# Kernel optimization log

Measured on AMD Instinct MI355X. Metric: run time of the kernel, lower is better.

## Reference

```python
import jax, jax.numpy as jnp
import numpy as np

B, D, L, T, K = 16, 256, 256, 1000, 3
DW, DC = 4, 2  # dim_w, dim_c
CH = 8         # ConvSwishBlock out channels (10 = 1 start + 1 end + 8)


def swish(x):
    return x * jax.nn.sigmoid(x)


def setup_inputs() -> dict:
    key = jax.random.key(0)
    ks = jax.random.split(key, 12)
    # durations ~ U[1,6] per phone -> sum ~ 3.5*L ~ 896 <= T
    durations = 1.0 + 5.0 * jax.random.uniform(ks[0], (B, L), dtype=jnp.float32)
    phoneme = jax.random.normal(ks[1], (B, D, L), dtype=jnp.float32)
    # True = padded phone position
    phone_len = L - (jnp.arange(B) % 4) * 16
    phoneme_mask = (jnp.arange(L)[None, :] >= phone_len[:, None])[:, None, :]
    durations = jnp.where(phoneme_mask[:, 0, :], 0.0, durations)
    s = 0.02
    p = {
        'proj_w_W': s * jax.random.normal(ks[2], (D, D)), 'proj_w_b': jnp.zeros((D,)),
        'conv_w_W': s * jax.random.normal(ks[3], (CH, D, K)), 'conv_w_b': jnp.zeros((CH,)),
        'mlp_w_W': s * jax.random.normal(ks[4], (2 + CH, DW)), 'mlp_w_b': jnp.zeros((DW,)),
        'lin_w_W': s * jax.random.normal(ks[5], (D * DW, D)), 'lin_w_b': jnp.zeros((D,)),
        'proj_c_W': s * jax.random.normal(ks[6], (D, D)), 'proj_c_b': jnp.zeros((D,)),
        'conv_c_W': s * jax.random.normal(ks[7], (CH, D, K)), 'conv_c_b': jnp.zeros((CH,)),
        'mlp_c_W': s * jax.random.normal(ks[8], (2 + CH, DC)), 'mlp_c_b': jnp.zeros((DC,)),
        'lin_c_W': s * jax.random.normal(ks[9], (DW * DC, D)), 'lin_c_b': jnp.zeros((D,)),
    }
    return {'durations': durations, 'phoneme': phoneme, 'phoneme_mask': phoneme_mask, **p}


def _conv_branch(x, phone_pad, projW, projb, convW, convb):
    # x: (B, D, L). 1x1 conv projection, then K-wide 'same' conv to CH channels, swish, mask.
    x = jnp.einsum('od,bdl->bol', projW, x) + projb[None, :, None]
    h = jax.lax.conv_general_dilated(x, convW, (1,), 'SAME',
                                     dimension_numbers=('NCH', 'OIH', 'NCH'))
    h = swish(h + convb[None, :, None])
    h = jnp.where(phone_pad[:, None, :], 0.0, h)
    return h.transpose(0, 2, 1)  # (B, L, CH)


def _forward(durations, phoneme, phoneme_mask,
             proj_w_W, proj_w_b, conv_w_W, conv_w_b, mlp_w_W, mlp_w_b, lin_w_W, lin_w_b,
             proj_c_W, proj_c_b, conv_c_W, conv_c_b, mlp_c_W, mlp_c_b, lin_c_W, lin_c_b):
    phone_pad = phoneme_mask[:, 0, :]                       # (B, L) True = pad
    frame_len = jnp.clip(jnp.round(jnp.sum(durations, -1)), 0, T).astype(jnp.int32)
    frame_pad = jnp.arange(T)[None, :] >= frame_len[:, None]  # (B, T) True = pad
    attn_pad = frame_pad[:, :, None] | phone_pad[:, None, :]  # (B, T, L)

    sd = jnp.cumsum(durations, -1)                          # (B, L) cumulative end times
    sk = sd - durations                                     # (B, L) start times
    t = jnp.arange(1, T + 1, dtype=durations.dtype)
    S = jnp.where(attn_pad, 0.0, t[None, :, None] - sk[:, None, :])                    # (B,T,L)
    E = jnp.where(attn_pad, 0.0, jnp.broadcast_to(sd[:, None, :], attn_pad.shape)
                  - sk[:, None, :])                                                    # (B,T,L)

    # W branch: per-(frame, phone) attention weights over phones
    h_w = _conv_branch(phoneme, phone_pad, proj_w_W, proj_w_b, conv_w_W, conv_w_b)     # (B,L,CH)
    feat_w = jnp.concatenate(
        [S[..., None], E[..., None], jnp.broadcast_to(h_w[:, None], (B, T, L, CH))], -1)
    w = swish(feat_w @ mlp_w_W + mlp_w_b)                   # (B, T, L, DW)
    w = jnp.where(phone_pad[:, None, :, None], -jnp.inf, w)
    w = jax.nn.softmax(w, axis=2)                           # softmax over phones
    w = jnp.where(frame_pad[:, :, None, None], 0.0, w)

    # C branch: auxiliary per-(frame, phone) context
    h_c = _conv_branch(phoneme, phone_pad, proj_c_W, proj_c_b, conv_c_W, conv_c_b)
    feat_c = jnp.concatenate(
        [S[..., None], E[..., None], jnp.broadcast_to(h_c[:, None], (B, T, L, CH))], -1)
    c = swish(feat_c @ mlp_c_W + mlp_c_b)                   # (B, T, L, DC)

    # combine: wh = einsum over phones with phoneme features, wc with c matrix
    wh = jnp.einsum('btnq,bnh->btqh', w, phoneme.transpose(0, 2, 1))  # (B,T,DW,D)
    wh = wh.reshape(B, T, DW * D) @ lin_w_W + lin_w_b                 # (B,T,D)
    wc = jnp.einsum('btnq,btnp->btqp', w, c)                          # (B,T,DW,DC)
    wc = wc.reshape(B, T, DW * DC) @ lin_c_W + lin_c_b                # (B,T,D)
    return wh + wc


def reference(durations, phoneme, phoneme_mask,
              proj_w_W, proj_w_b, conv_w_W, conv_w_b, mlp_w_W, mlp_w_b, lin_w_W, lin_w_b,
              proj_c_W, proj_c_b, conv_c_W, conv_c_b, mlp_c_W, mlp_c_b, lin_c_W, lin_c_b):
    return _forward(durations, phoneme, phoneme_mask,
                    proj_w_W, proj_w_b, conv_w_W, conv_w_b, mlp_w_W, mlp_w_b, lin_w_W, lin_w_b,
                    proj_c_W, proj_c_b, conv_c_W, conv_c_b, mlp_c_W, mlp_c_b, lin_c_W, lin_c_b)
```

## Files before the change

### kernel.cpp

```cpp
#include <hip/hip_runtime.h>


typedef short v8s __attribute__((ext_vector_type(8)));
typedef _Float16 v8h __attribute__((ext_vector_type(8)));
typedef float f4 __attribute__((ext_vector_type(4)));

__device__ __forceinline__ float bf2f(unsigned short h) {
  return __uint_as_float(((unsigned int)h) << 16);
}
__device__ __forceinline__ unsigned short f2bf(float f) {
  unsigned int u = __float_as_uint(f);
  u = (u + 0x7FFFu + ((u >> 16) & 1u)) >> 16;
  return (unsigned short)u;
}
__device__ __forceinline__ float swishf(float x) {
  return x * __builtin_amdgcn_rcpf(1.f + __expf(-x));
}

__global__ __launch_bounds__(256) void k_prep(
    const float* __restrict__ dur, const float* __restrict__ ph,
    const float* __restrict__ liWw,
    const float* __restrict__ cvWw, const float* __restrict__ pjWw,
    const float* __restrict__ pjbw,
    const float* __restrict__ cvWc, const float* __restrict__ pjWc,
    const float* __restrict__ pjbc,
    float* __restrict__ sk, int* __restrict__ frame_len,
    unsigned short* __restrict__ Mb, float* __restrict__ bK,
    unsigned short* __restrict__ LWT, unsigned short* __restrict__ phT) {
  __shared__ float sm[32 * 33];
  int blk = blockIdx.x, tid = threadIdx.x;
  if (blk < 16) {
    int b = blk, l = tid;
    float d = dur[b * 256 + l];
    sm[l] = d;
    __syncthreads();
    for (int off = 1; off < 256; off <<= 1) {
      float v = (l >= off) ? sm[l - off] : 0.f;
      __syncthreads();
      sm[l] += v;
      __syncthreads();
    }
    sk[b * 256 + l] = sm[l] - d;
    if (l == 255) {
      int fl = (int)rintf(sm[255]);
      frame_len[b] = min(max(fl, 0), 1000);
    }
  } else if (blk < 64) {
    int x = blk - 16;
    int br = x / 24, ck = x % 24;
    int ch = ck / 3, k = ck % 3;
    const float* convW = br ? cvWc : cvWw;
    const float* projW = br ? pjWc : pjWw;
    const float* projb = br ? pjbc : pjbw;
    int d = tid;
    float acc = 0.f;
    for (int o = 0; o < 256; o++)
      acc += convW[ch * 768 + o * 3 + k] * projW[o * 256 + d];
    Mb[(br * 24 + ck) * 256 + d] = f2bf(acc);
    if (d == 0) {
      float bb = 0.f;
      for (int o = 0; o < 256; o++)
        bb += convW[ch * 768 + o * 3 + k] * projb[o];
      bK[br * 24 + ck] = bb;
    }
  } else if (blk < 320) {
    int idx = blk - 64;
    int kt = idx & 31, ot = idx >> 5;
    int tx = tid & 31, ty = tid >> 5;
#pragma unroll
    for (int r = 0; r < 4; r++) {
      int row = ty + r * 8;
      sm[row * 33 + tx] = liWw[(size_t)(kt * 32 + row) * 256 + ot * 32 + tx];
    }
    __syncthreads();
#pragma unroll
    for (int r = 0; r < 4; r++) {
      int row = ty + r * 8;
      LWT[(size_t)(ot * 32 + row) * 1024 + kt * 32 + tx] =
          f2bf(sm[tx * 33 + row]);
    }
  } else {
    int idx = blk - 320;
    int ht = idx & 7, lt = (idx >> 3) & 7, b = idx >> 6;
    int tx = tid & 31, ty = tid >> 5;
#pragma unroll
    for (int r = 0; r < 4; r++) {
      int row = ty + r * 8;
      sm[row * 33 + tx] =
          ph[(size_t)b * 65536 + (size_t)(ht * 32 + row) * 256 + lt * 32 + tx];
    }
    __syncthreads();
#pragma unroll
    for (int r = 0; r < 4; r++) {
      int row = ty + r * 8;
      phT[(size_t)b * 65536 + (size_t)(lt * 32 + row) * 256 + ht * 32 + tx] =
          f2bf(sm[tx * 33 + row]);
    }
  }
}

__global__ __launch_bounds__(256) void k_convG(
    const unsigned short* __restrict__ phT, const unsigned short* __restrict__ Mb,
    const float* __restrict__ bK, const float* __restrict__ cvbw,
    const float* __restrict__ cvbc, const float* __restrict__ dur,
    const unsigned short* __restrict__ LWT,
    float* __restrict__ hw, float* __restrict__ hc,
    _Float16* __restrict__ G) {
  __shared__ __align__(16) char smem[50176];
  int blk = blockIdx.x;
  int tid = threadIdx.x, wave = tid >> 6, lane = tid & 63;
  int quad = lane >> 4, col = lane & 15;
  if (blk < 16) {
    float* C = (float*)smem;
    int b = blk;
    int l0 = wave * 64;
    const unsigned short* Ab = phT + (size_t)b * 65536;
    f4 acc[4][3] = {};
#pragma unroll
    for (int k0 = 0; k0 < 256; k0 += 32) {
      v8s af[4], bf[3];
#pragma unroll
      for (int lt = 0; lt < 4; lt++)
        af[lt] = *(const v8s*)(Ab + (size_t)(l0 + lt * 16 + col) * 256 + k0 + quad * 8);
#pragma unroll
      for (int ct = 0; ct < 3; ct++)
        bf[ct] = *(const v8s*)(Mb + (size_t)(ct * 16 + col) * 256 + k0 + quad * 8);
#pragma unroll
      for (int lt = 0; lt < 4; lt++)
#pragma unroll
        for (int ct = 0; ct < 3; ct++)
          acc[lt][ct] = __builtin_amdgcn_mfma_f32_16x16x32_bf16(af[lt], bf[ct],
                                                                acc[lt][ct], 0, 0, 0);
    }
#pragma unroll
    for (int lt = 0; lt < 4; lt++)
#pragma unroll
      for (int ct = 0; ct < 3; ct++)
#pragma unroll
        for (int r = 0; r < 4; r++)
          C[(l0 + lt * 16 + quad * 4 + r) * 49 + ct * 16 + col] = acc[lt][ct][r];
    __syncthreads();
    int l = tid;
    float dv = dur[b * 256 + l];
    bool vld = (dv != 0.f);
#pragma unroll
    for (int br = 0; br < 2; br++) {
      const float* convb = br ? cvbc : cvbw;
      float* dst = br ? hc : hw;
#pragma unroll
      for (int ch = 0; ch < 8; ch++) {
        int ck = br * 24 + ch * 3;
        float v = convb[ch] + bK[ck + 1] + C[l * 49 + ck + 1];
        if (l > 0) v += bK[ck + 0] + C[(l - 1) * 49 + ck + 0];
        if (l < 255) v += bK[ck + 2] + C[(l + 1) * 49 + ck + 2];
        v = swishf(v);
        dst[((size_t)(b * 256 + l)) * 8 + ch] = vld ? v : 0.f;
      }
    }
  } else {
    int idx = blk - 16;
    int x = idx & 7, q = (idx >> 3) & 3, b = idx >> 5;
    int o0 = (x >> 1) * 64, l0 = (x & 1) * 128;
    unsigned short* Asm = (unsigned short*)smem;
    unsigned short* Bsm = Asm + 64 * 40;
    int arow = wave * 16 + (lane >> 2);
    int aseg = lane & 3;
    const unsigned short* Ag = LWT + (size_t)(o0 + arow) * 1024 + q * 256 + aseg * 8;
    unsigned short* Al = Asm + arow * 40 + aseg * 8;
    int brow = wave * 32 + (lane >> 2);
    const unsigned short* Bg0 =
        phT + (size_t)b * 65536 + (size_t)(l0 + brow) * 256 + aseg * 8;
    const unsigned short* Bg1 = Bg0 + 16 * 256;
    unsigned short* Bl0 = Bsm + brow * 40 + aseg * 8;
    unsigned short* Bl1 = Bl0 + 16 * 40;
    int wm = (wave & 1) * 32, wn = (wave >> 1) * 64;
    f4 acc[2][4] = {};
    uint4 ra = *(const uint4*)Ag;
    uint4 rb0 = *(const uint4*)Bg0;
    uint4 rb1 = *(const uint4*)Bg1;
    for (int k0 = 0; k0 < 256; k0 += 32) {
      __syncthreads();
      *(uint4*)Al = ra;
      *(uint4*)Bl0 = rb0;
      *(uint4*)Bl1 = rb1;
      __syncthreads();
      if (k0 + 32 < 256) {
        ra = *(const uint4*)(Ag + k0 + 32);
        rb0 = *(const uint4*)(Bg0 + k0 + 32);
        rb1 = *(const uint4*)(Bg1 + k0 + 32);
      }
      v8s af[2], bf[4];
#pragma unroll
      for (int mt = 0; mt < 2; mt++)
        af[mt] = *(const v8s*)(Asm + (wm + mt * 16 + col) * 40 + quad * 8);
#pragma unroll
      for (int nt = 0; nt < 4; nt++)
        bf[nt] = *(const v8s*)(Bsm + (wn + nt * 16 + col) * 40 + quad * 8);
#pragma unroll
      for (int mt = 0; mt < 2; mt++)
#pragma unroll
        for (int nt = 0; nt < 4; nt++)
          acc[mt][nt] = __builtin_amdgcn_mfma_f32_16x16x32_bf16(af[mt], bf[nt],
                                                                acc[mt][nt], 0, 0, 0);
    }
#pragma unroll
    for (int mt = 0; mt < 2; mt++)
#pragma unroll
      for (int nt = 0; nt < 4; nt++)
#pragma unroll
        for (int r = 0; r < 4; r++) {
          int orow = o0 + wm + mt * 16 + quad * 4 + r;
          int lcol = l0 + wn + nt * 16 + col;
          G[(size_t)b * 262144 + (size_t)orow * 1024 + q * 256 + lcol] =
              (_Float16)acc[mt][nt][r];
        }
  }
}

__global__ __launch_bounds__(256) void k_fuse(
    const _Float16* __restrict__ G,
    const float* __restrict__ dur, const float* __restrict__ sk,
    const int* __restrict__ frame_len,
    const float* __restrict__ hw, const float* __restrict__ hc,
    const float* __restrict__ mlpWw, const float* __restrict__ mlpbw,
    const float* __restrict__ mlpWc, const float* __restrict__ mlpbc,
    const float* __restrict__ lwb, const float* __restrict__ lcb,
    const float* __restrict__ LC, float* __restrict__ out) {
  __shared__ __align__(16) _Float16 Et[2][32][264];
  __shared__ __align__(16) float4 Lbw4[256];
  __shared__ __align__(16) float4 Laux4[256];
  __shared__ float4 wredM[4];
  __shared__ float invL[32 * 4];
  __shared__ float wcL[32 * 8];

  int blk = blockIdx.x;
  int b = (blk & 7) * 2 + ((blk >> 3) & 1);
  int tile = blk >> 4;
  int t0 = tile * 32;
  int tid = threadIdx.x, wave = tid >> 6, lane = tid & 63;
  int quad = lane >> 4, col = lane & 15;

  {
    int l = tid;
    float4 a0 = *(const float4*)&hw[((size_t)(b * 256 + l)) * 8];
    float4 a1 = *(const float4*)&hw[((size_t)(b * 256 + l)) * 8 + 4];
    float4 c0 = *(const float4*)&hc[((size_t)(b * 256 + l)) * 8];
    float4 c1 = *(const float4*)&hc[((size_t)(b * 256 + l)) * 8 + 4];
    float hwv[8] = {a0.x, a0.y, a0.z, a0.w, a1.x, a1.y, a1.z, a1.w};
    float hcv[8] = {c0.x, c0.y, c0.z, c0.w, c1.x, c1.y, c1.z, c1.w};
    float dl = dur[b * 256 + l];
    float skl = sk[b * 256 + l];
    float msk = (dl != 0.f) ? 1.f : 0.f;
    float A[4];
#pragma unroll
    for (int q = 0; q < 4; q++) {
      float a = mlpbw[q] + dl * mlpWw[4 + q] - skl * mlpWw[q];
#pragma unroll
      for (int ch = 0; ch < 8; ch++) a += hwv[ch] * mlpWw[(2 + ch) * 4 + q];
      A[q] = (msk != 0.f) ? a : -1e30f;
    }
    float bb0 = mlpbc[0] + dl * mlpWc[2] - skl * mlpWc[0];
    float bb1 = mlpbc[1] + dl * mlpWc[3] - skl * mlpWc[1];
#pragma unroll
    for (int ch = 0; ch < 8; ch++) {
      bb0 += hcv[ch] * mlpWc[(2 + ch) * 2 + 0];
      bb1 += hcv[ch] * mlpWc[(2 + ch) * 2 + 1];
    }
    float4 Av = {A[0], A[1], A[2], A[3]};
    Lbw4[l] = Av;
    float4 xv = {bb0, bb1, msk, 0.f};
    Laux4[l] = xv;
    float m0 = A[0], m1 = A[1], m2 = A[2], m3 = A[3];
#pragma unroll
    for (int off = 1; off < 64; off <<= 1) {
      m0 = fmaxf(m0, __shfl_xor(m0, off));
      m1 = fmaxf(m1, __shfl_xor(m1, off));
      m2 = fmaxf(m2, __shfl_xor(m2, off));
      m3 = fmaxf(m3, __shfl_xor(m3, off));
    }
    if (lane == 0) {
      float4 mv = {m0, m1, m2, m3};
      wredM[wave] = mv;
    }
  }
  __syncthreads();
  float4 W0 = wredM[0], W1 = wredM[1], W2 = wredM[2], W3 = wredM[3];
  float maxA[4] = {fmaxf(fmaxf(W0.x, W1.x), fmaxf(W2.x, W3.x)),
                   fmaxf(fmaxf(W0.y, W1.y), fmaxf(W2.y, W3.y)),
                   fmaxf(fmaxf(W0.z, W1.z), fmaxf(W2.z, W3.z)),
                   fmaxf(fmaxf(W0.w, W1.w), fmaxf(W2.w, W3.w))};

  int fl = frame_len[b];
  int tg = tid >> 5, seg = tid & 31;
  float mw0[4] = {mlpWw[0], mlpWw[1], mlpWw[2], mlpWw[3]};
  float mc0 = mlpWc[0], mc1 = mlpWc[1];
  float tp1v[4], tS0[4], tS1[4];
  bool livev[4];
#pragma unroll
  for (int ti = 0; ti < 4; ti++) {
    int t = t0 + tg * 4 + ti;
    livev[ti] = (t < fl);
    tp1v[ti] = (float)(t + 1);
    tS0[ti] = tp1v[ti] * mc0;
    tS1[ti] = tp1v[ti] * mc1;
  }

  int wn = wave * 64;
  f4 accF[2][4] = {};
  const _Float16* Gb = G + (size_t)b * 262144;

#pragma unroll
  for (int pp = 0; pp < 2; pp++) {
    if (pp) __syncthreads();
    int qa = pp * 2;
    float mm[4][2];
#pragma unroll
    for (int ti = 0; ti < 4; ti++) {
      mm[ti][0] = livev[ti] ? fmaxf(maxA[qa] + tp1v[ti] * mw0[qa], 0.f) : 1e30f;
      mm[ti][1] = livev[ti] ? fmaxf(maxA[qa + 1] + tp1v[ti] * mw0[qa + 1], 0.f) : 1e30f;
    }
    float s[4][2] = {}, pw0[4][2] = {}, pw1[4][2] = {};
    for (int jj = 0; jj < 8; jj++) {
      int l = jj * 32 + seg;
      float4 A4 = Lbw4[l];
      float4 ax = Laux4[l];
      float Aa = pp ? A4.z : A4.x;
      float Ab = pp ? A4.w : A4.y;
#pragma unroll
      for (int ti = 0; ti < 4; ti++) {
        float tp1 = tp1v[ti];
        float za = Aa + tp1 * mw0[qa];
        float zb = Ab + tp1 * mw0[qa + 1];
        float ea = __expf(swishf(za) - mm[ti][0]) * ax.z;
        float eb = __expf(swishf(zb) - mm[ti][1]) * ax.z;
        float cp0 = swishf(ax.x + tS0[ti]);
        float cp1 = swishf(ax.y + tS1[ti]);
        s[ti][0] += ea;  pw0[ti][0] += ea * cp0;  pw1[ti][0] += ea * cp1;
        s[ti][1] += eb;  pw0[ti][1] += eb * cp0;  pw1[ti][1] += eb * cp1;
        Et[0][tg * 4 + ti][l] = (_Float16)ea;
        Et[1][tg * 4 + ti][l] = (_Float16)eb;
      }
    }
#pragma unroll
    for (int off = 1; off < 32; off <<= 1) {
#pragma unroll
      for (int ti = 0; ti < 4; ti++) {
#pragma unroll
        for (int e2 = 0; e2 < 2; e2++) {
          s[ti][e2] += __shfl_xor(s[ti][e2], off);
          pw0[ti][e2] += __shfl_xor(pw0[ti][e2], off);
          pw1[ti][e2] += __shfl_xor(pw1[ti][e2], off);
        }
      }
    }
    if (seg == 0) {
#pragma unroll
      for (int ti = 0; ti < 4; ti++) {
        int row = tg * 4 + ti;
#pragma unroll
        for (int e2 = 0; e2 < 2; e2++) {
          int qq = qa + e2;
          float iv = livev[ti] ? __builtin_amdgcn_rcpf(s[ti][e2]) : 0.f;
          invL[row * 4 + qq] = iv;
          wcL[row * 8 + qq * 2 + 0] = pw0[ti][e2] * iv;
          wcL[row * 8 + qq * 2 + 1] = pw1[ti][e2] * iv;
        }
      }
    }
    __syncthreads();
#pragma unroll
    for (int e2 = 0; e2 < 2; e2++) {
      int qq = qa + e2;
      f4 accq[2][4] = {};
#pragma unroll
      for (int k0 = 0; k0 < 256; k0 += 32) {
        v8h af[2], bf[4];
#pragma unroll
        for (int mt = 0; mt < 2; mt++)
          af[mt] = *(const v8h*)&Et[e2][mt * 16 + col][k0 + quad * 8];
#pragma unroll
        for (int nt = 0; nt < 4; nt++)
          bf[nt] = *(const v8h*)(Gb + (size_t)(wn + nt * 16 + col) * 1024 +
                                 qq * 256 + k0 + quad * 8);
#pragma unroll
        for (int mt = 0; mt < 2; mt++)
#pragma unroll
          for (int nt = 0; nt < 4; nt++)
            accq[mt][nt] = __builtin_amdgcn_mfma_f32_16x16x32_f16(af[mt], bf[nt],
                                                                  accq[mt][nt], 0, 0, 0);
      }
#pragma unroll
      for (int mt = 0; mt < 2; mt++)
#pragma unroll
        for (int r = 0; r < 4; r++) {
          float iv = invL[(mt * 16 + quad * 4 + r) * 4 + qq];
#pragma unroll
          for (int nt = 0; nt < 4; nt++)
            accF[mt][nt][r] += accq[mt][nt][r] * iv;
        }
    }
  }

#pragma unroll
  for (int nt = 0; nt < 4; nt++) {
    int oc = wn + nt * 16 + col;
    float bias = lwb[oc] + lcb[oc];
    float lc8[8];
#pragma unroll
    for (int jj = 0; jj < 8; jj++) lc8[jj] = LC[jj * 256 + oc];
#pragma unroll
    for (int mt = 0; mt < 2; mt++)
#pragma unroll
      for (int r = 0; r < 4; r++) {
        int lr = mt * 16 + quad * 4 + r;
        int trow = t0 + lr;
        if (trow < 1000) {
          float v = accF[mt][nt][r] + bias;
#pragma unroll
          for (int jj = 0; jj < 8; jj++) v = fmaf(wcL[lr * 8 + jj], lc8[jj], v);
          out[((size_t)(b * 1000 + trow)) * 256 + oc] = v;
        }
      }
  }
}

extern "C" void kernel_launch(void* const* d_in, const int* in_sizes, int n_in,
                              void* d_out, int out_size, void* d_ws, size_t ws_size,
                              hipStream_t stream) {
  const float* dur  = (const float*)d_in[0];
  const float* ph   = (const float*)d_in[1];
  const float* pjWw = (const float*)d_in[3];
  const float* pjbw = (const float*)d_in[4];
  const float* cvWw = (const float*)d_in[5];
  const float* cvbw = (const float*)d_in[6];
  const float* mlWw = (const float*)d_in[7];
  const float* mlbw = (const float*)d_in[8];
  const float* liWw = (const float*)d_in[9];
  const float* libw = (const float*)d_in[10];
  const float* pjWc = (const float*)d_in[11];
  const float* pjbc = (const float*)d_in[12];
  const float* cvWc = (const float*)d_in[13];
  const float* cvbc = (const float*)d_in[14];
  const float* mlWc = (const float*)d_in[15];
  const float* mlbc = (const float*)d_in[16];
  const float* liWc = (const float*)d_in[17];
  const float* libc = (const float*)d_in[18];
  float* out = (float*)d_out;

  float* f = (float*)d_ws;
  size_t o = 0;
  float* sk = f + o;            o += 4096;
  int* fl = (int*)(f + o);      o += 16;
  float* bK = f + o;            o += 64;
  unsigned short* Mb = (unsigned short*)(f + o); o += 6144;
  float* hw = f + o;            o += 16 * 256 * 8;
  float* hc = f + o;            o += 16 * 256 * 8;
  _Float16* G = (_Float16*)(f + o);              o += 2097152;
  unsigned short* phT = (unsigned short*)(f + o); o += 524288;
  unsigned short* LWT = (unsigned short*)(f + o); o += 131072;

  k_prep<<<1344, 256, 0, stream>>>(dur, ph, liWw, cvWw, pjWw, pjbw, cvWc, pjWc,
                                   pjbc, sk, fl, Mb, bK, LWT, phT);
  k_convG<<<528, 256, 0, stream>>>(phT, Mb, bK, cvbw, cvbc, dur, LWT, hw, hc, G);
  k_fuse<<<512, 256, 0, stream>>>(G, dur, sk, fl, hw, hc, mlWw, mlbw, mlWc,
                                  mlbc, libw, libc, liWc, out);
}
```

Baseline: 193.5 us.

## Halve fuse time tile to 16 frames and drop LDS staging in G GEMM

The fuse kernel now processes 16 time frames per block instead of 32, doubling the grid to 1008 blocks and adding an occupancy hint of 4 blocks per CU. The goal is to spread the dominant fused softmax/GEMM work across more CUs. The G-producing GEMM drops its shared-memory double-buffer staging and reads operands directly from global memory with larger 64x64 per-wave tiles, cutting its grid from 528 to 272 blocks. The trade-off is that each G column block is now re-read by twice as many fuse blocks, and the direct global loads in the G GEMM rely on cache reuse rather than LDS.

After: 205.3 us. 6.1% more time.

```diff
diff --git a/kernel.cpp b/kernel.cpp
--- a/kernel.cpp
+++ b/kernel.cpp
@@ -106,12 +106,11 @@
     const unsigned short* __restrict__ LWT,
     float* __restrict__ hw, float* __restrict__ hc,
     _Float16* __restrict__ G) {
-  __shared__ __align__(16) char smem[50176];
+  __shared__ __align__(16) float C[256 * 49];
   int blk = blockIdx.x;
   int tid = threadIdx.x, wave = tid >> 6, lane = tid & 63;
   int quad = lane >> 4, col = lane & 15;
   if (blk < 16) {
-    float* C = (float*)smem;
     int b = blk;
     int l0 = wave * 64;
     const unsigned short* Ab = phT + (size_t)b * 65536;
@@ -159,65 +158,48 @@
     }
   } else {
     int idx = blk - 16;
-    int x = idx & 7, q = (idx >> 3) & 3, b = idx >> 5;
-    int o0 = (x >> 1) * 64, l0 = (x & 1) * 128;
-    unsigned short* Asm = (unsigned short*)smem;
-    unsigned short* Bsm = Asm + 64 * 40;
-    int arow = wave * 16 + (lane >> 2);
-    int aseg = lane & 3;
-    const unsigned short* Ag = LWT + (size_t)(o0 + arow) * 1024 + q * 256 + aseg * 8;
-    unsigned short* Al = Asm + arow * 40 + aseg * 8;
-    int brow = wave * 32 + (lane >> 2);
-    const unsigned short* Bg0 =
-        phT + (size_t)b * 65536 + (size_t)(l0 + brow) * 256 + aseg * 8;
-    const unsigned short* Bg1 = Bg0 + 16 * 256;
-    unsigned short* Bl0 = Bsm + brow * 40 + aseg * 8;
-    unsigned short* Bl1 = Bl0 + 16 * 40;
-    int wm = (wave & 1) * 32, wn = (wave >> 1) * 64;
-    f4 acc[2][4] = {};
-    uint4 ra = *(const uint4*)Ag;
-    uint4 rb0 = *(const uint4*)Bg0;
-    uint4 rb1 = *(const uint4*)Bg1;
+    int b = idx >> 4;
+    int sub = idx & 15;
+    int q = sub >> 2, quadr = sub & 3;
+    int mo = (quadr >> 1) * 128, nl = (quadr & 1) * 128;
+    int wm = (wave & 1) * 64, wn = (wave >> 1) * 64;
+    const unsigned short* Ag = LWT + (size_t)q * 256;
+    const unsigned short* Bg = phT + (size_t)b * 65536;
+    f4 acc[4][4] = {};
+#pragma unroll
     for (int k0 = 0; k0 < 256; k0 += 32) {
-      __syncthreads();
-      *(uint4*)Al = ra;
-      *(uint4*)Bl0 = rb0;
-      *(uint4*)Bl1 = rb1;
-      __syncthreads();
-      if (k0 + 32 < 256) {
-        ra = *(const uint4*)(Ag + k0 + 32);
-        rb0 = *(const uint4*)(Bg0 + k0 + 32);
-        rb1 = *(const uint4*)(Bg1 + k0 + 32);
-      }
-      v8s af[2], bf[4];
-#pragma unroll
-      for (int mt = 0; mt < 2; mt++)
-        af[mt] = *(const v8s*)(Asm + (wm + mt * 16 + col) * 40 + quad * 8);
+      v8s af[4], bf[4];
+#pragma unroll
+      for (int mt = 0; mt < 4; mt++)
+        af[mt] = *(const v8s*)(Ag + (size_t)(mo + wm + mt * 16 + col) * 1024 +
+                               k0 + quad * 8);
 #pragma unroll
       for (int nt = 0; nt < 4; nt++)
-        bf[nt] = *(const v8s*)(Bsm + (wn + nt * 16 + col) * 40 + quad * 8);
-#pragma unroll
-      for (int mt = 0; mt < 2; mt++)
+        bf[nt] = *(const v8s*)(Bg + (size_t)(nl + wn + nt * 16 + col) * 256 +
+                               k0 + quad * 8);
+#pragma unroll
+      for (int mt = 0; mt < 4; mt++)
 #pragma unroll
         for (int nt = 0; nt < 4; nt++)
           acc[mt][nt] = __builtin_amdgcn_mfma_f32_16x16x32_bf16(af[mt], bf[nt],
                                                                 acc[mt][nt], 0, 0, 0);
     }
-#pragma unroll
-    for (int mt = 0; mt < 2; mt++)
-#pragma unroll
-      for (int nt = 0; nt < 4; nt++)
-#pragma unroll
-        for (int r = 0; r < 4; r++) {
-          int orow = o0 + wm + mt * 16 + quad * 4 + r;
-          int lcol = l0 + wn + nt * 16 + col;
-          G[(size_t)b * 262144 + (size_t)orow * 1024 + q * 256 + lcol] =
-              (_Float16)acc[mt][nt][r];
+    _Float16* Gb = G + (size_t)b * 262144 + q * 256;
+#pragma unroll
+    for (int mt = 0; mt < 4; mt++)
+#pragma unroll
+      for (int r = 0; r < 4; r++) {
+        int orow = mo + wm + mt * 16 + quad * 4 + r;
+#pragma unroll
+        for (int nt = 0; nt < 4; nt++) {
+          int lcol = nl + wn + nt * 16 + col;
+          Gb[(size_t)orow * 1024 + lcol] = (_Float16)acc[mt][nt][r];
         }
-  }
-}
-
-__global__ __launch_bounds__(256) void k_fuse(
+      }
+  }
+}
+
+__global__ __launch_bounds__(256, 4) void k_fuse(
     const _Float16* __restrict__ G,
     const float* __restrict__ dur, const float* __restrict__ sk,
     const int* __restrict__ frame_len,
@@ -226,17 +208,17 @@
     const float* __restrict__ mlpWc, const float* __restrict__ mlpbc,
     const float* __restrict__ lwb, const float* __restrict__ lcb,
     const float* __restrict__ LC, float* __restrict__ out) {
-  __shared__ __align__(16) _Float16 Et[2][32][264];
+  __shared__ __align__(16) _Float16 Et[2][16][264];
   __shared__ __align__(16) float4 Lbw4[256];
   __shared__ __align__(16) float4 Laux4[256];
   __shared__ float4 wredM[4];
-  __shared__ float invL[32 * 4];
-  __shared__ float wcL[32 * 8];
+  __shared__ float invL[16 * 4];
+  __shared__ float wcL[16 * 8];
 
   int blk = blockIdx.x;
   int b = (blk & 7) * 2 + ((blk >> 3) & 1);
   int tile = blk >> 4;
-  int t0 = tile * 32;
+  int t0 = tile * 16;
   int tid = threadIdx.x, wave = tid >> 6, lane = tid & 63;
   int quad = lane >> 4, col = lane & 15;
 
@@ -294,11 +276,11 @@
   int tg = tid >> 5, seg = tid & 31;
   float mw0[4] = {mlpWw[0], mlpWw[1], mlpWw[2], mlpWw[3]};
   float mc0 = mlpWc[0], mc1 = mlpWc[1];
-  float tp1v[4], tS0[4], tS1[4];
-  bool livev[4];
-#pragma unroll
-  for (int ti = 0; ti < 4; ti++) {
-    int t = t0 + tg * 4 + ti;
+  float tp1v[2], tS0[2], tS1[2];
+  bool livev[2];
+#pragma unroll
+  for (int ti = 0; ti < 2; ti++) {
+    int t = t0 + tg + 8 * ti;
     livev[ti] = (t < fl);
     tp1v[ti] = (float)(t + 1);
     tS0[ti] = tp1v[ti] * mc0;
@@ -306,20 +288,20 @@
   }
 
   int wn = wave * 64;
-  f4 accF[2][4] = {};
+  f4 accF[4] = {};
   const _Float16* Gb = G + (size_t)b * 262144;
 
 #pragma unroll
   for (int pp = 0; pp < 2; pp++) {
     if (pp) __syncthreads();
     int qa = pp * 2;
-    float mm[4][2];
-#pragma unroll
-    for (int ti = 0; ti < 4; ti++) {
+    float mm[2][2];
+#pragma unroll
+    for (int ti = 0; ti < 2; ti++) {
       mm[ti][0] = livev[ti] ? fmaxf(maxA[qa] + tp1v[ti] * mw0[qa], 0.f) : 1e30f;
       mm[ti][1] = livev[ti] ? fmaxf(maxA[qa + 1] + tp1v[ti] * mw0[qa + 1], 0.f) : 1e30f;
     }
-    float s[4][2] = {}, pw0[4][2] = {}, pw1[4][2] = {};
+    float s[2][2] = {}, pw0[2][2] = {}, pw1[2][2] = {};
     for (int jj = 0; jj < 8; jj++) {
       int l = jj * 32 + seg;
       float4 A4 = Lbw4[l];
@@ -327,7 +309,7 @@
       float Aa = pp ? A4.z : A4.x;
       float Ab = pp ? A4.w : A4.y;
 #pragma unroll
-      for (int ti = 0; ti < 4; ti++) {
+      for (int ti = 0; ti < 2; ti++) {
         float tp1 = tp1v[ti];
         float za = Aa + tp1 * mw0[qa];
         float zb = Ab + tp1 * mw0[qa + 1];
@@ -337,26 +319,25 @@
         float cp1 = swishf(ax.y + tS1[ti]);
         s[ti][0] += ea;  pw0[ti][0] += ea * cp0;  pw1[ti][0] += ea * cp1;
         s[ti][1] += eb;  pw0[ti][1] += eb * cp0;  pw1[ti][1] += eb * cp1;
-        Et[0][tg * 4 + ti][l] = (_Float16)ea;
-        Et[1][tg * 4 + ti][l] = (_Float16)eb;
+        Et[0][tg + 8 * ti][l] = (_Float16)ea;
+        Et[1][tg + 8 * ti][l] = (_Float16)eb;
       }
     }
 #pragma unroll
     for (int off = 1; off < 32; off <<= 1) {
 #pragma unroll
-      for (int ti = 0; ti < 4; ti++) {
+      for (int ti = 0; ti < 2; ti++)
 #pragma unroll
         for (int e2 = 0; e2 < 2; e2++) {
           s[ti][e2] += __shfl_xor(s[ti][e2], off);
           pw0[ti][e2] += __shfl_xor(pw0[ti][e2], off);
           pw1[ti][e2] += __shfl_xor(pw1[ti][e2], off);
         }
-      }
     }
     if (seg == 0) {
 #pragma unroll
-      for (int ti = 0; ti < 4; ti++) {
-        int row = tg * 4 + ti;
+      for (int ti = 0; ti < 2; ti++) {
+        int row = tg + 8 * ti;
 #pragma unroll
         for (int e2 = 0; e2 < 2; e2++) {
           int qq = qa + e2;
@@ -371,33 +352,26 @@
 #pragma unroll
     for (int e2 = 0; e2 < 2; e2++) {
       int qq = qa + e2;
-      f4 accq[2][4] = {};
+      f4 accq[4] = {};
 #pragma unroll
       for (int k0 = 0; k0 < 256; k0 += 32) {
-        v8h af[2], bf[4];
-#pragma unroll
-        for (int mt = 0; mt < 2; mt++)
-          af[mt] = *(const v8h*)&Et[e2][mt * 16 + col][k0 + quad * 8];
+        v8h af = *(const v8h*)&Et[e2][col][k0 + quad * 8];
+        v8h bf[4];
 #pragma unroll
         for (int nt = 0; nt < 4; nt++)
           bf[nt] = *(const v8h*)(Gb + (size_t)(wn + nt * 16 + col) * 1024 +
                                  qq * 256 + k0 + quad * 8);
 #pragma unroll
-        for (int mt = 0; mt < 2; mt++)
-#pragma unroll
-          for (int nt = 0; nt < 4; nt++)
-            accq[mt][nt] = __builtin_amdgcn_mfma_f32_16x16x32_f16(af[mt], bf[nt],
-                                                                  accq[mt][nt], 0, 0, 0);
-      }
-#pragma unroll
-      for (int mt = 0; mt < 2; mt++)
-#pragma unroll
-        for (int r = 0; r < 4; r++) {
-          float iv = invL[(mt * 16 + quad * 4 + r) * 4 + qq];
-#pragma unroll
-          for (int nt = 0; nt < 4; nt++)
-            accF[mt][nt][r] += accq[mt][nt][r] * iv;
-        }
+        for (int nt = 0; nt < 4; nt++)
+          accq[nt] = __builtin_amdgcn_mfma_f32_16x16x32_f16(af, bf[nt],
+                                                            accq[nt], 0, 0, 0);
+      }
+#pragma unroll
+      for (int r = 0; r < 4; r++) {
+        float iv = invL[(quad * 4 + r) * 4 + qq];
+#pragma unroll
+        for (int nt = 0; nt < 4; nt++) accF[nt][r] += accq[nt][r] * iv;
+      }
     }
   }
 
@@ -409,18 +383,16 @@
 #pragma unroll
     for (int jj = 0; jj < 8; jj++) lc8[jj] = LC[jj * 256 + oc];
 #pragma unroll
-    for (int mt = 0; mt < 2; mt++)
-#pragma unroll
-      for (int r = 0; r < 4; r++) {
-        int lr = mt * 16 + quad * 4 + r;
-        int trow = t0 + lr;
-        if (trow < 1000) {
-          float v = accF[mt][nt][r] + bias;
-#pragma unroll
-          for (int jj = 0; jj < 8; jj++) v = fmaf(wcL[lr * 8 + jj], lc8[jj], v);
-          out[((size_t)(b * 1000 + trow)) * 256 + oc] = v;
-        }
-      }
+    for (int r = 0; r < 4; r++) {
+      int lr = quad * 4 + r;
+      int trow = t0 + lr;
+      if (trow < 1000) {
+        float v = accF[nt][r] + bias;
+#pragma unroll
+        for (int jj = 0; jj < 8; jj++) v = fmaf(wcL[lr * 8 + jj], lc8[jj], v);
+        out[((size_t)(b * 1000 + trow)) * 256 + oc] = v;
+      }
+    }
   }
 }
 
@@ -461,7 +433,7 @@
 
   k_prep<<<1344, 256, 0, stream>>>(dur, ph, liWw, cvWw, pjWw, pjbw, cvWc, pjWc,
                                    pjbc, sk, fl, Mb, bK, LWT, phT);
-  k_convG<<<528, 256, 0, stream>>>(phT, Mb, bK, cvbw, cvbc, dur, LWT, hw, hc, G);
-  k_fuse<<<512, 256, 0, stream>>>(G, dur, sk, fl, hw, hc, mlWw, mlbw, mlWc,
-                                  mlbc, libw, libc, liWc, out);
-}
+  k_convG<<<272, 256, 0, stream>>>(phT, Mb, bK, cvbw, cvbc, dur, LWT, hw, hc, G);
+  k_fuse<<<1008, 256, 0, stream>>>(G, dur, sk, fl, hw, hc, mlWw, mlbw, mlWc,
+                                   mlbc, libw, libc, liWc, out);
+}
```
